# Kernel tuning notes

Measured on AMD Instinct MI355X. Metric: run time of the kernel, lower is better.

## Reference

```python
import jax, jax.numpy as jnp
import numpy as np

B, C, H, W = 64, 3, 512, 512
WEIGHT = 1.0


def _high_freq_mask(h, w):
    m = np.ones((h, w), dtype=np.float32)
    ch, cw = h // 2, w // 2
    m[ch - h // 8:ch + h // 8, cw - w // 8:cw + w // 8] = 0.0
    return jnp.asarray(m), float(m.sum())


def setup_inputs() -> dict:
    key = jax.random.key(0)
    k1, k2 = jax.random.split(key)
    # images in [-1, 1]
    generated = jax.random.uniform(k1, (B, C, H, W), dtype=jnp.float32, minval=-1.0, maxval=1.0)
    target = jax.random.uniform(k2, (B, C, H, W), dtype=jnp.float32, minval=-1.0, maxval=1.0)
    return {"generated": generated, "target": target}


def _to_gray01(x):
    # (B,3,H,W) in [-1,1] -> (B,H,W) grayscale in [0,1]
    g = x[:, 0] * 0.299 + x[:, 1] * 0.587 + x[:, 2] * 0.114
    return (g + 1.0) * 0.5


def _high_freq_psd(gray):
    # gray: (B,H,W) float32
    h, w = gray.shape[-2:]
    mask, count = _high_freq_mask(h, w)
    fft = jnp.fft.fftshift(jnp.fft.fft2(gray), axes=(-2, -1))  # (B,H,W) complex64
    psd = jnp.real(fft) ** 2 + jnp.imag(fft) ** 2
    psd_log = jnp.log10(psd + 1e-10)
    # mean over high-frequency (masked) region; count is static
    return jnp.sum(psd_log * mask, axis=(-2, -1)) / count  # (B,)


def reference(generated, target):
    psd_gen = _high_freq_psd(_to_gray01(generated))
    psd_tgt = _high_freq_psd(_to_gray01(target))
    loss = jnp.mean(jnp.abs(psd_gen - psd_tgt))  # F.l1_loss
    return WEIGHT * loss
```

## Files before the change

### kernel.cpp

```cpp
#include <hip/hip_runtime.h>
#include <math.h>

#ifndef M_PI
#define M_PI 3.14159265358979323846
#endif


__device__ __forceinline__ float2 cmulf(float2 a, float2 b) {
    return make_float2(fmaf(a.x, b.x, -(a.y * b.y)), fmaf(a.x, b.y, a.y * b.x));
}
__device__ __forceinline__ float2 caddf(float2 a, float2 b){ return make_float2(a.x+b.x, a.y+b.y); }
__device__ __forceinline__ float2 csubf(float2 a, float2 b){ return make_float2(a.x-b.x, a.y-b.y); }

__device__ __forceinline__ void lds_order() {
    __builtin_amdgcn_sched_barrier(0);
}

__device__ __forceinline__ void dft8(float2 v[8]) {
    const float S = 0.70710678118654752440f;
    float2 a0=caddf(v[0],v[4]), a1=caddf(v[1],v[5]), a2=caddf(v[2],v[6]), a3=caddf(v[3],v[7]);
    float2 b0=csubf(v[0],v[4]);
    float2 t1=csubf(v[1],v[5]);
    float2 t2=csubf(v[2],v[6]);
    float2 t3=csubf(v[3],v[7]);
    float2 b1=make_float2(S*(t1.x+t1.y), S*(t1.y-t1.x));
    float2 b2=make_float2(t2.y, -t2.x);
    float2 b3=make_float2(S*(t3.y-t3.x), -S*(t3.x+t3.y));
    float2 c0=caddf(a0,a2), c1=caddf(a1,a3), c2=csubf(a0,a2);
    float2 u3=csubf(a1,a3); float2 c3=make_float2(u3.y,-u3.x);
    float2 d0=caddf(b0,b2), d1=caddf(b1,b3), d2=csubf(b0,b2);
    float2 w3=csubf(b1,b3); float2 d3=make_float2(w3.y,-w3.x);
    v[0]=caddf(c0,c1); v[4]=csubf(c0,c1);
    v[2]=caddf(c2,c3); v[6]=csubf(c2,c3);
    v[1]=caddf(d0,d1); v[5]=csubf(d0,d1);
    v[3]=caddf(d2,d3); v[7]=csubf(d2,d3);
}

__device__ __forceinline__ void twapply(float2 v[8], float2 w) {
    const float2 w2 = cmulf(w,  w);
    const float2 w3 = cmulf(w2, w);
    const float2 w4 = cmulf(w2, w2);
    const float2 w5 = cmulf(w2, w3);
    const float2 w6 = cmulf(w3, w3);
    const float2 w7 = cmulf(w4, w3);
    v[1] = cmulf(v[1], w);
    v[2] = cmulf(v[2], w2);
    v[3] = cmulf(v[3], w3);
    v[4] = cmulf(v[4], w4);
    v[5] = cmulf(v[5], w5);
    v[6] = cmulf(v[6], w6);
    v[7] = cmulf(v[7], w7);
}

__device__ __forceinline__ void fft512_reg(float2 v[8], float2* __restrict__ W,
                                           const float2* __restrict__ twg, int lane) {
    dft8(v);
    twapply(v, twg[lane]);
#pragma unroll
    for (int c = 0; c < 8; ++c) W[(c<<6) + ((lane + 2*c)&63)] = v[c];
    lds_order();
    {
        const int c = lane>>3, p = lane&7, base = c<<6, off = p + 2*c;
#pragma unroll
        for (int bb = 0; bb < 8; ++bb) v[bb] = W[base + (((bb<<3) + off)&63)];
    }
    lds_order();
    dft8(v);
    twapply(v, twg[(lane&7)<<3]);
    {
        const int c = lane>>3, p = lane&7, base = c<<6, r2 = 2*c;
#pragma unroll
        for (int d = 0; d < 8; ++d) W[base + (((d<<3) + (p^d) + r2)&63)] = v[d];
    }
    lds_order();
    {
        const int c = lane>>3, d = lane&7, base = c<<6, off = (d<<3) + 2*c;
#pragma unroll
        for (int p = 0; p < 8; ++p) v[p] = W[base + ((off + (p^d))&63)];
    }
    lds_order();
    dft8(v);
}

__global__ void twiddle_kernel(float2* __restrict__ tw) {
    const int k = threadIdx.x;
    const double ang = -2.0 * M_PI * (double)k / 512.0;
    tw[k] = make_float2((float)cos(ang), (float)sin(ang));
}

__global__ __launch_bounds__(512, 4)
void row_fft_kernel(const float* __restrict__ gen, const float* __restrict__ tgt,
                    const float2* __restrict__ twg, float2* __restrict__ scratch,
                    int b0) {
    __shared__ float2 SBUF[8 * 512];
    const int tid = threadIdx.x, wave = tid>>6, lane = tid&63;
    const int img = blockIdx.x>>6, rg = blockIdx.x&63;
    const int b = b0 + img, r = (rg<<3) + wave;

    const size_t rowoff = ((size_t)b * 3 * 512 + r) * 512;
    const float* gR = gen + rowoff; const float* gG = gR + 262144; const float* gB = gG + 262144;
    const float* tR = tgt + rowoff; const float* tG = tR + 262144; const float* tB = tG + 262144;

    float2 v[8];
#pragma unroll
    for (int a = 0; a < 8; ++a) {
        const int idx = (a<<6) + lane;
        const float gg = fmaf(0.299f, gR[idx], fmaf(0.587f, gG[idx], fmaf(0.114f, gB[idx], 1.0f))) * 0.5f;
        const float tt = fmaf(0.299f, tR[idx], fmaf(0.587f, tG[idx], fmaf(0.114f, tB[idx], 1.0f))) * 0.5f;
        v[a] = make_float2(gg, tt);
    }

    float2* W = SBUF + (wave<<9);
    fft512_reg(v, W, twg, lane);

#pragma unroll
    for (int e = 0; e < 8; ++e) {
        const int col = (e<<6) + lane;
        W[(col + (wave<<3)) & 511] = v[e];
    }
    __syncthreads();

    const size_t obase = (size_t)img << 18;
    const int r0 = rg<<3;
#pragma unroll
    for (int it = 0; it < 8; ++it) {
        const int col = (tid>>3) + (it<<6);
        const int j = tid&7;
        scratch[obase + ((size_t)col<<9) + r0 + j] = SBUF[(j<<9) + ((col + (j<<3)) & 511)];
    }
}

__global__ __launch_bounds__(128, 4)
void col_fft_reduce_kernel(const float2* __restrict__ scratch,
                           const float2* __restrict__ twg,
                           double* __restrict__ accum, int b0) {
    __shared__ float2 SBUF[2 * 512];
    const int tid = threadIdx.x, wave = tid>>6, lane = tid&63;
    const int img = blockIdx.x>>8, t = blockIdx.x&255;
    const int b = b0 + img;
    const int kx = (t==0) ? (wave<<8) : (wave ? 512-t : t);
    const int col = ((kx>>6)<<6) + ((kx&7)<<3) + ((kx>>3)&7);
    float2* W = SBUF + (wave<<9);

    const float2* src = scratch + ((size_t)img<<18) + ((size_t)col<<9);
    float2 v[8];
#pragma unroll
    for (int a = 0; a < 8; ++a) v[a] = src[(a<<6) + lane];

    fft512_reg(v, W, twg, lane);

    const int cc = lane>>3, dd = lane&7;
#pragma unroll
    for (int e = 0; e < 8; ++e) W[cc + (dd<<3) + (e<<6)] = v[e];
    __syncthreads();

    const float2* pbuf = (t==0) ? W : (SBUF + ((1-wave)<<9));
    const bool kxin = (kx < 64) || (kx >= 448);

    double sg = 0.0, st = 0.0;
#pragma unroll
    for (int e = 0; e < 8; ++e) {
        const int ky = cc + (dd<<3) + (e<<6);
        if (kxin && ((ky < 64) || (ky >= 448))) continue;
        const float2 F1 = v[e];
        const float2 F2 = pbuf[(512 - ky) & 511];
        const float ar = 0.5f*(F1.x + F2.x), ai = 0.5f*(F1.y - F2.y);
        const float br = 0.5f*(F1.y + F2.y), bi = 0.5f*(F2.x - F1.x);
        const float pg = fmaf(ar, ar, ai*ai) + 1e-10f;
        const float pt = fmaf(br, br, bi*bi) + 1e-10f;
        sg += (double)log10f(pg);
        st += (double)log10f(pt);
    }
#pragma unroll
    for (int off = 32; off; off >>= 1) {
        sg += __shfl_down(sg, off);
        st += __shfl_down(st, off);
    }
    if (lane == 0) {
        atomicAdd(&accum[b], sg);
        atomicAdd(&accum[64 + b], st);
    }
}

__global__ void finalize_kernel(const double* __restrict__ accum,
                                float* __restrict__ out) {
    const int lane = threadIdx.x;
    double d = fabs(accum[lane] - accum[64 + lane]) * (1.0 / 245760.0);
#pragma unroll
    for (int off = 32; off; off >>= 1) d += __shfl_down(d, off);
    if (lane == 0) out[0] = (float)(d * (1.0 / 64.0));
}

extern "C" void kernel_launch(void* const* d_in, const int* in_sizes, int n_in,
                              void* d_out, int out_size, void* d_ws, size_t ws_size,
                              hipStream_t stream) {
    (void)in_sizes; (void)n_in; (void)out_size;
    const float* gen = (const float*)d_in[0];
    const float* tgt = (const float*)d_in[1];
    float*  out     = (float*)d_out;
    float2* tw      = (float2*)d_ws;
    double* accum   = (double*)((char*)d_ws + 2048);
    float2* scratch = (float2*)((char*)d_ws + 4096);

    const size_t per_img = (size_t)512 * 512 * sizeof(float2);
    const size_t avail = (ws_size > 4096) ? (ws_size - 4096) : 0;
    int chunk = 64;
    while (chunk > 1 && (size_t)chunk * per_img > avail) chunk >>= 1;

    hipMemsetAsync(accum, 0, 128 * sizeof(double), stream);
    twiddle_kernel<<<1, 256, 0, stream>>>(tw);
    for (int b0 = 0; b0 < 64; b0 += chunk) {
        row_fft_kernel<<<dim3(chunk * 64), dim3(512), 0, stream>>>(gen, tgt, tw, scratch, b0);
        col_fft_reduce_kernel<<<dim3(chunk * 256), dim3(128), 0, stream>>>(scratch, tw, accum, b0);
    }
    finalize_kernel<<<1, 64, 0, stream>>>(accum, out);
}
```

Measured before the change: 579.0 us.

## Pair conjugate columns within one wave and replace atomics with partial-sum reduction

Each wave now computes both column FFTs for kx and 512-kx itself and reads the mirrored spectrum from its own LDS slice. Previously two waves each did one FFT and exchanged results through shared memory with a block barrier. Blocks grow to four waves, and per-wave double atomics are replaced by a partial-sum buffer reduced in a new kernel, which also removes the memset. The intent is to drop __syncthreads and atomic contention and to raise per-wave ILP. The costs are higher register pressure from holding two 8-element vectors plus two reversed copies, and one extra kernel launch.

```diff
diff --git a/kernel.cpp b/kernel.cpp
--- a/kernel.cpp
+++ b/kernel.cpp
@@ -130,55 +130,106 @@
     }
 }
 
-__global__ __launch_bounds__(128, 4)
+__device__ __forceinline__ void accum_psd(float2 F1, float2 F2, double& sg, double& st) {
+    const float ar = 0.5f*(F1.x + F2.x), ai = 0.5f*(F1.y - F2.y);
+    const float br = 0.5f*(F1.y + F2.y), bi = 0.5f*(F2.x - F1.x);
+    const float pg = fmaf(ar, ar, ai*ai) + 1e-10f;
+    const float pt = fmaf(br, br, bi*bi) + 1e-10f;
+    sg += (double)log10f(pg);
+    st += (double)log10f(pt);
+}
+
+__global__ __launch_bounds__(256, 4)
 void col_fft_reduce_kernel(const float2* __restrict__ scratch,
                            const float2* __restrict__ twg,
-                           double* __restrict__ accum, int b0) {
-    __shared__ float2 SBUF[2 * 512];
+                           double2* __restrict__ partial, int b0) {
+    __shared__ float2 SBUF[4 * 512];
     const int tid = threadIdx.x, wave = tid>>6, lane = tid&63;
-    const int img = blockIdx.x>>8, t = blockIdx.x&255;
+    const int gw = (blockIdx.x<<2) + wave;
+    const int img = gw>>8, t = gw&255;
     const int b = b0 + img;
-    const int kx = (t==0) ? (wave<<8) : (wave ? 512-t : t);
-    const int col = ((kx>>6)<<6) + ((kx&7)<<3) + ((kx>>3)&7);
+    const int kxA = t;
+    const int kxB = (t == 0) ? 256 : 512 - t;
+    const int colA = ((kxA>>6)<<6) + ((kxA&7)<<3) + ((kxA>>3)&7);
+    const int colB = ((kxB>>6)<<6) + ((kxB&7)<<3) + ((kxB>>3)&7);
     float2* W = SBUF + (wave<<9);
 
-    const float2* src = scratch + ((size_t)img<<18) + ((size_t)col<<9);
-    float2 v[8];
-#pragma unroll
-    for (int a = 0; a < 8; ++a) v[a] = src[(a<<6) + lane];
-
-    fft512_reg(v, W, twg, lane);
+    const float2* srcA = scratch + ((size_t)img<<18) + ((size_t)colA<<9);
+    const float2* srcB = scratch + ((size_t)img<<18) + ((size_t)colB<<9);
+    float2 va[8], vb[8];
+#pragma unroll
+    for (int a = 0; a < 8; ++a) va[a] = srcA[(a<<6) + lane];
+#pragma unroll
+    for (int a = 0; a < 8; ++a) vb[a] = srcB[(a<<6) + lane];
+
+    fft512_reg(va, W, twg, lane);
 
     const int cc = lane>>3, dd = lane&7;
-#pragma unroll
-    for (int e = 0; e < 8; ++e) W[cc + (dd<<3) + (e<<6)] = v[e];
-    __syncthreads();
-
-    const float2* pbuf = (t==0) ? W : (SBUF + ((1-wave)<<9));
-    const bool kxin = (kx < 64) || (kx >= 448);
+    const int kyb = cc + (dd<<3);
+
+#pragma unroll
+    for (int e = 0; e < 8; ++e) W[kyb + (e<<6)] = va[e];
+    lds_order();
+    float2 aRev[8];
+#pragma unroll
+    for (int e = 0; e < 8; ++e) aRev[e] = W[(512 - (kyb + (e<<6))) & 511];
+    lds_order();
+
+    fft512_reg(vb, W, twg, lane);
+
+#pragma unroll
+    for (int e = 0; e < 8; ++e) W[kyb + (e<<6)] = vb[e];
+    lds_order();
+    float2 bRev[8];
+#pragma unroll
+    for (int e = 0; e < 8; ++e) bRev[e] = W[(512 - (kyb + (e<<6))) & 511];
+    lds_order();
+
+    const bool kxinA = (t < 64);
+    const bool kxinB = (t >= 1 && t <= 64);
 
     double sg = 0.0, st = 0.0;
-#pragma unroll
-    for (int e = 0; e < 8; ++e) {
-        const int ky = cc + (dd<<3) + (e<<6);
-        if (kxin && ((ky < 64) || (ky >= 448))) continue;
-        const float2 F1 = v[e];
-        const float2 F2 = pbuf[(512 - ky) & 511];
-        const float ar = 0.5f*(F1.x + F2.x), ai = 0.5f*(F1.y - F2.y);
-        const float br = 0.5f*(F1.y + F2.y), bi = 0.5f*(F2.x - F1.x);
-        const float pg = fmaf(ar, ar, ai*ai) + 1e-10f;
-        const float pt = fmaf(br, br, bi*bi) + 1e-10f;
-        sg += (double)log10f(pg);
-        st += (double)log10f(pt);
+    if (t == 0) {
+#pragma unroll
+        for (int e = 0; e < 8; ++e) {
+            if (!(kxinA && (e == 0 || e == 7))) accum_psd(va[e], aRev[e], sg, st);
+            accum_psd(vb[e], bRev[e], sg, st);
+        }
+    } else {
+#pragma unroll
+        for (int e = 0; e < 8; ++e) {
+            if (!(kxinA && (e == 0 || e == 7))) accum_psd(va[e], bRev[e], sg, st);
+            if (!(kxinB && (e == 0 || e == 7))) accum_psd(vb[e], aRev[e], sg, st);
+        }
     }
 #pragma unroll
     for (int off = 32; off; off >>= 1) {
         sg += __shfl_down(sg, off);
         st += __shfl_down(st, off);
     }
-    if (lane == 0) {
-        atomicAdd(&accum[b], sg);
-        atomicAdd(&accum[64 + b], st);
+    if (lane == 0) partial[((size_t)b<<8) + t] = make_double2(sg, st);
+}
+
+__global__ __launch_bounds__(256)
+void reduce_partial_kernel(const double2* __restrict__ partial,
+                           double* __restrict__ accum) {
+    __shared__ double2 red[4];
+    const int img = blockIdx.x, tid = threadIdx.x, wave = tid>>6, lane = tid&63;
+    const double2 p = partial[((size_t)img<<8) + tid];
+    double sg = p.x, st = p.y;
+#pragma unroll
+    for (int off = 32; off; off >>= 1) {
+        sg += __shfl_down(sg, off);
+        st += __shfl_down(st, off);
+    }
+    if (lane == 0) red[wave] = make_double2(sg, st);
+    __syncthreads();
+    if (tid == 0) {
+        double SG = 0.0, ST = 0.0;
+#pragma unroll
+        for (int w = 0; w < 4; ++w) { SG += red[w].x; ST += red[w].y; }
+        accum[img] = SG;
+        accum[64 + img] = ST;
     }
 }
 
@@ -197,21 +248,22 @@
     (void)in_sizes; (void)n_in; (void)out_size;
     const float* gen = (const float*)d_in[0];
     const float* tgt = (const float*)d_in[1];
-    float*  out     = (float*)d_out;
-    float2* tw      = (float2*)d_ws;
-    double* accum   = (double*)((char*)d_ws + 2048);
-    float2* scratch = (float2*)((char*)d_ws + 4096);
+    float*   out     = (float*)d_out;
+    float2*  tw      = (float2*)d_ws;
+    double*  accum   = (double*)((char*)d_ws + 2048);
+    double2* partial = (double2*)((char*)d_ws + 4096);
+    float2*  scratch = (float2*)((char*)d_ws + 266240);
 
     const size_t per_img = (size_t)512 * 512 * sizeof(float2);
-    const size_t avail = (ws_size > 4096) ? (ws_size - 4096) : 0;
+    const size_t avail = (ws_size > 266240) ? (ws_size - 266240) : 0;
     int chunk = 64;
     while (chunk > 1 && (size_t)chunk * per_img > avail) chunk >>= 1;
 
-    hipMemsetAsync(accum, 0, 128 * sizeof(double), stream);
     twiddle_kernel<<<1, 256, 0, stream>>>(tw);
     for (int b0 = 0; b0 < 64; b0 += chunk) {
         row_fft_kernel<<<dim3(chunk * 64), dim3(512), 0, stream>>>(gen, tgt, tw, scratch, b0);
-        col_fft_reduce_kernel<<<dim3(chunk * 256), dim3(128), 0, stream>>>(scratch, tw, accum, b0);
-    }
+        col_fft_reduce_kernel<<<dim3(chunk * 64), dim3(256), 0, stream>>>(scratch, tw, partial, b0);
+    }
+    reduce_partial_kernel<<<dim3(64), dim3(256), 0, stream>>>(partial, accum);
     finalize_kernel<<<1, 64, 0, stream>>>(accum, out);
 }
```

Measured after the change: 499.2 us. 1.16x faster.
